# Optimization experiments

Hardware: AMD Instinct MI355X
Metric: run time of the kernel (lower is better)

## Reference

```python
import jax, jax.numpy as jnp
import numpy as np

NEG = -1e9  # effectively -inf for masked logits, grad-safe

def apply_rope(t, cos, sin):
    # t: [b, H, S, D]; cos/sin: [S, D] -> rotate-half RoPE
    d = t.shape[-1]
    t1, t2 = t[..., : d // 2], t[..., d // 2 :]
    rot = jnp.concatenate([-t2, t1], axis=-1)
    return t * cos[None, None] + rot * sin[None, None]


def setup_inputs() -> dict:
    key = jax.random.key(0)
    ks = jax.random.split(key, 8)
    b, S, d_in = 1, 4096, 2048
    H, G, D = 16, 4, 128
    d_out = H * D
    sc = 1.0 / np.sqrt(d_in)
    x = jax.random.normal(ks[0], (b, S, d_in), dtype=jnp.float32)
    # causal mask: True = masked (future positions)
    mask = jnp.triu(jnp.ones((S, S), dtype=bool), k=1)
    inv = 1.0 / (10000.0 ** (jnp.arange(0, D, 2, dtype=jnp.float32) / D))
    ang = jnp.arange(S, dtype=jnp.float32)[:, None] * inv[None, :]  # [S, D/2]
    ang = jnp.concatenate([ang, ang], axis=-1)                      # [S, D]
    cos, sin = jnp.cos(ang), jnp.sin(ang)
    Wq = jax.random.normal(ks[1], (d_out, d_in), dtype=jnp.float32) * sc
    Wk = jax.random.normal(ks[2], (G * D, d_in), dtype=jnp.float32) * sc
    Wv = jax.random.normal(ks[3], (G * D, d_in), dtype=jnp.float32) * sc
    Wo = jax.random.normal(ks[4], (d_in, d_out), dtype=jnp.float32) * sc
    return {"x": x, "mask": mask, "cos": cos, "sin": sin,
            "Wq": Wq, "Wk": Wk, "Wv": Wv, "Wo": Wo}


def reference(x, mask, cos, sin, Wq, Wk, Wv, Wo):
    b, S, d_in = x.shape
    G = Wk.shape[0] // cos.shape[-1]          # num_kv_groups
    D = cos.shape[-1]                          # head_dim
    H = Wq.shape[0] // D                       # num_heads
    n = H // G                                 # group_size
    q = (x @ Wq.T).reshape(b, S, H, D).transpose(0, 2, 1, 3)   # [b,H,S,D]
    k = (x @ Wk.T).reshape(b, S, G, D).transpose(0, 2, 1, 3)   # [b,G,S,D]
    v = (x @ Wv.T).reshape(b, S, G, D).transpose(0, 2, 1, 3)
    q = apply_rope(q, cos, sin)
    k = apply_rope(k, cos, sin)
    # GQA: group heads instead of repeat_interleave (head h -> group h // n)
    qg = q.reshape(b, G, n, S, D)
    scores = jnp.einsum('bgnqd,bgkd->bgnqk', qg, k)            # [b,G,n,S,S]
    scores = jnp.where(mask[None, None, None], NEG, scores)
    w = jax.nn.softmax(scores / np.sqrt(D), axis=-1)
    ctx = jnp.einsum('bgnqk,bgkd->bgnqd', w, v)                # [b,G,n,S,D]
    ctx = ctx.reshape(b, H, S, D).transpose(0, 2, 1, 3).reshape(b, S, H * D)
    return ctx @ Wo.T
```

## Files before the change

### kernel.cpp

```cpp
#include <hip/hip_runtime.h>

typedef __attribute__((ext_vector_type(8))) short bf16x8;
typedef __attribute__((ext_vector_type(4))) short bf16x4;
typedef __attribute__((ext_vector_type(8))) unsigned short u16x8;
typedef __attribute__((ext_vector_type(4))) float f32x4;

__device__ __forceinline__ unsigned short f2b(float f) {
  unsigned int u = __builtin_bit_cast(unsigned int, f);
  u += 0x7FFFu + ((u >> 16) & 1u);
  return (unsigned short)(u >> 16);
}
__device__ __forceinline__ float b2f(unsigned short h) {
  return __builtin_bit_cast(float, ((unsigned int)h) << 16);
}

__device__ __forceinline__ f32x4 mfma16x16x16(bf16x4 a, bf16x4 b, f32x4 c) {
#if __has_builtin(__builtin_amdgcn_mfma_f32_16x16x16bf16_1k)
  return __builtin_amdgcn_mfma_f32_16x16x16bf16_1k(a, b, c, 0, 0, 0);
#else
  asm volatile("v_mfma_f32_16x16x16_bf16 %0, %1, %2, %0" : "+v"(c) : "v"(a), "v"(b));
  return c;
#endif
}

#define AS1(p) (const __attribute__((address_space(1))) void*)(p)
#define AS3(p) (__attribute__((address_space(3))) void*)(p)

__global__ __launch_bounds__(256) void k_cvt(const float* __restrict__ in,
                                             unsigned short* __restrict__ out,
                                             float scale) {
  int i = blockIdx.x * 256 + threadIdx.x;
  const float4* p = (const float4*)in + (size_t)i * 2;
  float4 a = p[0], b = p[1];
  u16x8 r;
  r[0] = f2b(a.x * scale); r[1] = f2b(a.y * scale);
  r[2] = f2b(a.z * scale); r[3] = f2b(a.w * scale);
  r[4] = f2b(b.x * scale); r[5] = f2b(b.y * scale);
  r[6] = f2b(b.z * scale); r[7] = f2b(b.w * scale);
  *((u16x8*)out + i) = r;
}

__global__ __launch_bounds__(256) void k_rope(unsigned short* __restrict__ qk,
                                              const float* __restrict__ cosb,
                                              const float* __restrict__ sinb) {
  int tid = blockIdx.x * 256 + threadIdx.x;
  int oct = tid & 7;
  int hd  = (tid >> 3) % 20;
  int s   = (tid >> 3) / 20;
  unsigned short* p1 = qk + (size_t)s * 3072 + hd * 128 + oct * 8;
  unsigned short* p2 = p1 + 64;
  u16x8 a = *(const u16x8*)p1;
  u16x8 b = *(const u16x8*)p2;
  const float4* cp = (const float4*)(cosb + (size_t)s * 128 + oct * 8);
  const float4* sp = (const float4*)(sinb + (size_t)s * 128 + oct * 8);
  float4 c0 = cp[0], c1 = cp[1], s0 = sp[0], s1 = sp[1];
  float cs[8] = {c0.x,c0.y,c0.z,c0.w,c1.x,c1.y,c1.z,c1.w};
  float sn[8] = {s0.x,s0.y,s0.z,s0.w,s1.x,s1.y,s1.z,s1.w};
  u16x8 ra, rb;
#pragma unroll
  for (int j = 0; j < 8; ++j) {
    float av = b2f(a[j]), bv = b2f(b[j]);
    ra[j] = f2b(av * cs[j] - bv * sn[j]);
    rb[j] = f2b(bv * cs[j] + av * sn[j]);
  }
  *(u16x8*)p1 = ra;
  *(u16x8*)p2 = rb;
}

__global__ __launch_bounds__(256) void k_tr(const unsigned short* __restrict__ src,
                                            unsigned short* __restrict__ dst) {
  __shared__ unsigned short tile[64][72];
  const int bs = blockIdx.x, bc = blockIdx.y, t = threadIdx.x;
#pragma unroll
  for (int i = 0; i < 2; ++i) {
    int c8 = t + 256 * i;
    int row = c8 >> 3, cb = c8 & 7;
    u16x8 v = *(const u16x8*)(src + (size_t)(bs * 64 + row) * 3072 + 2560 + bc * 64 + cb * 8);
#pragma unroll
    for (int j = 0; j < 8; ++j) tile[row][cb * 8 + j] = v[j];
  }
  __syncthreads();
#pragma unroll
  for (int i = 0; i < 2; ++i) {
    int c8 = t + 256 * i;
    int crow = c8 >> 3, sb = c8 & 7;
    u16x8 v;
#pragma unroll
    for (int j = 0; j < 8; ++j) v[j] = tile[sb * 8 + j][crow];
    *(u16x8*)(dst + (size_t)(bc * 64 + crow) * 4096 + bs * 64 + sb * 8) = v;
  }
}

template <int OUTF32>
__global__ __launch_bounds__(256) void k_gemm_bt(
    const unsigned short* __restrict__ A, const unsigned short* __restrict__ B,
    void* __restrict__ C, int K, int lda, int ldb, int ldc) {
  __shared__ unsigned short As[128 * 64];
  __shared__ unsigned short Bs[128 * 64];
  const int t = threadIdx.x;
  const int lane = t & 63, w = t >> 6;
  const int wm = w >> 1, wn = w & 1;
  const int bn = blockIdx.x, bm = blockIdx.y;
  const unsigned short* Arow = A + (size_t)(bm * 128) * lda;
  const unsigned short* Brow = B + (size_t)(bn * 128) * ldb;

  f32x4 acc[4][4] = {};
  for (int kt = 0; kt < K; kt += 64) {
#pragma unroll
    for (int i = 0; i < 4; ++i) {
      int idx = i * 256 + t;
      int r = idx >> 3, blk = idx & 7;
      int sb = blk ^ (r & 7);
      __builtin_amdgcn_global_load_lds(AS1(Arow + (size_t)r * lda + kt + sb * 8),
                                       AS3(As + (i * 256 + w * 64) * 8), 16, 0, 0);
    }
#pragma unroll
    for (int i = 0; i < 4; ++i) {
      int idx = i * 256 + t;
      int r = idx >> 3, blk = idx & 7;
      int sb = blk ^ (r & 7);
      __builtin_amdgcn_global_load_lds(AS1(Brow + (size_t)r * ldb + kt + sb * 8),
                                       AS3(Bs + (i * 256 + w * 64) * 8), 16, 0, 0);
    }
    __syncthreads();
#pragma unroll
    for (int kk = 0; kk < 2; ++kk) {
      bf16x8 av[4], bv[4];
#pragma unroll
      for (int i = 0; i < 4; ++i) {
        int r = wm * 64 + i * 16 + (lane & 15);
        int off = (r * 128 + (kk * 32 + (lane >> 4) * 8) * 2) ^ ((r & 7) << 4);
        av[i] = *(const bf16x8*)((const char*)As + off);
      }
#pragma unroll
      for (int j = 0; j < 4; ++j) {
        int r = wn * 64 + j * 16 + (lane & 15);
        int off = (r * 128 + (kk * 32 + (lane >> 4) * 8) * 2) ^ ((r & 7) << 4);
        bv[j] = *(const bf16x8*)((const char*)Bs + off);
      }
#pragma unroll
      for (int i = 0; i < 4; ++i)
#pragma unroll
        for (int j = 0; j < 4; ++j)
          acc[i][j] = __builtin_amdgcn_mfma_f32_16x16x32_bf16(av[i], bv[j], acc[i][j], 0, 0, 0);
    }
    __syncthreads();
  }
#pragma unroll
  for (int i = 0; i < 4; ++i)
#pragma unroll
    for (int j = 0; j < 4; ++j)
#pragma unroll
      for (int r = 0; r < 4; ++r) {
        int m = bm * 128 + wm * 64 + i * 16 + (lane >> 4) * 4 + r;
        int n = bn * 128 + wn * 64 + j * 16 + (lane & 15);
        float v = acc[i][j][r];
        if (OUTF32) ((float*)C)[(size_t)m * ldc + n] = v;
        else        ((unsigned short*)C)[(size_t)m * ldc + n] = f2b(v);
      }
}

__device__ __forceinline__ void stage_k(const unsigned short* __restrict__ qk,
                                        unsigned short* __restrict__ dst,
                                        int kt, int g, int t, int w) {
#pragma unroll
  for (int i = 0; i < 4; ++i) {
    int idx = i * 256 + t;
    int r = idx >> 4, blk = idx & 15;
    int sb = (blk & 8) | ((blk ^ r) & 7);
    __builtin_amdgcn_global_load_lds(
        AS1(qk + (size_t)(kt * 64 + r) * 3072 + 2048 + g * 128 + sb * 8),
        AS3(dst + (i * 256 + w * 64) * 8), 16, 0, 0);
  }
}
__device__ __forceinline__ void stage_v(const unsigned short* __restrict__ vT,
                                        unsigned short* __restrict__ dst,
                                        int kt, int g, int t, int w) {
#pragma unroll
  for (int i = 0; i < 4; ++i) {
    int idx = i * 256 + t;
    int r = idx >> 3, blk = idx & 7;
    int sb = blk ^ (r & 7);
    __builtin_amdgcn_global_load_lds(
        AS1(vT + (size_t)(g * 128 + r) * 4096 + kt * 64 + sb * 8),
        AS3(dst + (i * 256 + w * 64) * 8), 16, 0, 0);
  }
}

__global__ __launch_bounds__(256, 2) void k_attn(const unsigned short* __restrict__ qk,
                                                 const unsigned short* __restrict__ vT,
                                                 unsigned short* __restrict__ ctx) {
  __shared__ unsigned short Ks[2][64 * 128];
  __shared__ unsigned short Vs[2][64 * 128];
  const int b = blockIdx.x, h = blockIdx.y, g = h >> 2;
  const int t = threadIdx.x, lane = t & 63, w = t >> 6;
  const int l15 = lane & 15, lq = lane >> 4;

  for (int ph = 0; ph < 2; ++ph) {
    const int qt = ph ? 63 - b : b;
    const int qg = qt * 64 + w * 16 + l15;

    bf16x8 aq[4];
    {
      const unsigned short* qb =
          qk + (size_t)(qt * 64 + w * 16 + l15) * 3072 + h * 128 + lq * 8;
#pragma unroll
      for (int sl = 0; sl < 4; ++sl) aq[sl] = *(const bf16x8*)(qb + sl * 32);
    }
    f32x4 o[8] = {};
    float lsum = 0.f;

    stage_k(qk, Ks[0], 0, g, t, w);
    stage_v(vT, Vs[0], 0, g, t, w);
    asm volatile("s_waitcnt vmcnt(0)" ::: "memory");
    __builtin_amdgcn_s_barrier();

    auto tile = [&](const unsigned short* Kb, const unsigned short* Vb,
                    int kt, bool maskT) {
      f32x4 st[4] = {};
      __builtin_amdgcn_s_setprio(1);
#pragma unroll
      for (int sl = 0; sl < 4; ++sl)
#pragma unroll
        for (int nt = 0; nt < 4; ++nt) {
          int key = nt * 16 + l15;
          int off = (key * 256 + sl * 64 + lq * 16) ^ ((key & 7) << 4);
          bf16x8 bk = *(const bf16x8*)((const char*)Kb + off);
          st[nt] = __builtin_amdgcn_mfma_f32_16x16x32_bf16(bk, aq[sl], st[nt], 0, 0, 0);
        }
      __builtin_amdgcn_s_setprio(0);

      bf16x4 pa[4];
#pragma unroll
      for (int nt = 0; nt < 4; ++nt)
#pragma unroll
        for (int r = 0; r < 4; ++r) {
          float p = __builtin_amdgcn_exp2f(st[nt][r]);
          if (maskT) {
            int key = kt * 64 + nt * 16 + lq * 4 + r;
            if (key > qg) p = 0.f;
          }
          lsum += p;
          unsigned int u = __builtin_bit_cast(unsigned int, p) + 0x8000u;
          pa[nt][r] = (short)(u >> 16);
        }

      __builtin_amdgcn_s_setprio(1);
#pragma unroll
      for (int nt = 0; nt < 4; ++nt)
#pragma unroll
        for (int dt = 0; dt < 8; ++dt) {
          int d = dt * 16 + l15;
          int off = (d * 128 + nt * 32 + lq * 8) ^ ((d & 7) << 4);
          bf16x4 vv = *(const bf16x4*)((const char*)Vb + off);
          o[dt] = mfma16x16x16(pa[nt], vv, o[dt]);
        }
      __builtin_amdgcn_s_setprio(0);
    };

    for (int kt = 0; kt < qt; ++kt) {
      const int cur = kt & 1;
      stage_k(qk, Ks[cur ^ 1], kt + 1, g, t, w);
      stage_v(vT, Vs[cur ^ 1], kt + 1, g, t, w);
      tile(Ks[cur], Vs[cur], kt, false);
      asm volatile("s_waitcnt vmcnt(0)" ::: "memory");
      __builtin_amdgcn_s_barrier();
    }
    {
      const int cur = qt & 1;
      tile(Ks[cur], Vs[cur], qt, true);
      __builtin_amdgcn_s_barrier();
    }

    float fs = lsum;
    fs += __shfl_xor(fs, 16);
    fs += __shfl_xor(fs, 32);
    float invq[4];
#pragma unroll
    for (int r = 0; r < 4; ++r) invq[r] = 1.f / __shfl(fs, lq * 4 + r);
#pragma unroll
    for (int dt = 0; dt < 8; ++dt)
#pragma unroll
      for (int r = 0; r < 4; ++r) {
        int q = qt * 64 + w * 16 + lq * 4 + r;
        int c = h * 128 + dt * 16 + l15;
        ctx[(size_t)q * 2048 + c] = f2b(o[dt][r] * invq[r]);
      }
  }
}

extern "C" void kernel_launch(void* const* d_in, const int* in_sizes, int n_in,
                              void* d_out, int out_size, void* d_ws, size_t ws_size,
                              hipStream_t stream) {
  const float* x    = (const float*)d_in[0];
  const float* cosb = (const float*)d_in[2];
  const float* sinb = (const float*)d_in[3];
  const float* Wq   = (const float*)d_in[4];
  const float* Wk   = (const float*)d_in[5];
  const float* Wv   = (const float*)d_in[6];
  const float* Wo   = (const float*)d_in[7];

  char* p = (char*)d_ws;
  unsigned short* xb   = (unsigned short*)p; p += (size_t)8388608 * 2;
  unsigned short* wqkv = (unsigned short*)p; p += (size_t)6291456 * 2;
  unsigned short* Wob  = (unsigned short*)p; p += (size_t)4194304 * 2;
  unsigned short* qkvb = (unsigned short*)p; p += (size_t)4096 * 3072 * 2;
  unsigned short* vTb  = (unsigned short*)p; p += (size_t)512 * 4096 * 2;
  unsigned short* ctx  = (unsigned short*)p; p += (size_t)4096 * 2048 * 2;
  if (ws_size < (size_t)(p - (char*)d_ws)) return;

  const float SC = 0.12751741f;

  k_cvt<<<4096, 256, 0, stream>>>(x,  xb, 1.f);
  k_cvt<<<2048, 256, 0, stream>>>(Wq, wqkv,           SC);
  k_cvt<<< 512, 256, 0, stream>>>(Wk, wqkv + 4194304, 1.f);
  k_cvt<<< 512, 256, 0, stream>>>(Wv, wqkv + 5242880, 1.f);
  k_cvt<<<2048, 256, 0, stream>>>(Wo, Wob, 1.f);

  k_gemm_bt<0><<<dim3(24, 32), 256, 0, stream>>>(xb, wqkv, qkvb, 2048, 2048, 2048, 3072);

  k_rope<<<2560, 256, 0, stream>>>(qkvb, cosb, sinb);
  k_tr<<<dim3(64, 8), 256, 0, stream>>>(qkvb, vTb);

  k_attn<<<dim3(32, 16), 256, 0, stream>>>(qkvb, vTb, ctx);

  k_gemm_bt<1><<<dim3(16, 32), 256, 0, stream>>>(ctx, Wob, d_out, 2048, 2048, 2048, 2048);
}
```

Before: 255.1 us.

## Single-buffer V in attention, raise occupancy, and merge small prep kernels

The attention kernel drops the double-buffered V tile. Each V tile is now loaded after the P·V step and overlapped only with the next tile's QK and softmax, with split waitcnt and barrier points. This frees LDS so launch bounds can be raised to three blocks per CU. Separately, the five fp32→bf16 conversion launches become one kernel, and RoPE plus the V transpose become one launch, cutting launch overhead. The trade-off is less latency hiding for V loads, while a 512-block grid may not fill the extra occupancy.

Measured after the change: 276.1 us. 8.2% more time.

```diff
diff --git a/kernel.cpp b/kernel.cpp
--- a/kernel.cpp
+++ b/kernel.cpp
@@ -26,10 +26,9 @@
 #define AS1(p) (const __attribute__((address_space(1))) void*)(p)
 #define AS3(p) (__attribute__((address_space(3))) void*)(p)
 
-__global__ __launch_bounds__(256) void k_cvt(const float* __restrict__ in,
-                                             unsigned short* __restrict__ out,
-                                             float scale) {
-  int i = blockIdx.x * 256 + threadIdx.x;
+__device__ __forceinline__ void cvt8(const float* __restrict__ in,
+                                     unsigned short* __restrict__ out,
+                                     int i, float scale) {
   const float4* p = (const float4*)in + (size_t)i * 2;
   float4 a = p[0], b = p[1];
   u16x8 r;
@@ -40,54 +39,71 @@
   *((u16x8*)out + i) = r;
 }
 
-__global__ __launch_bounds__(256) void k_rope(unsigned short* __restrict__ qk,
+__global__ __launch_bounds__(256) void k_cvt_all(
+    const float* __restrict__ x,  const float* __restrict__ Wq,
+    const float* __restrict__ Wk, const float* __restrict__ Wv,
+    const float* __restrict__ Wo, unsigned short* __restrict__ xb,
+    unsigned short* __restrict__ wqkv, unsigned short* __restrict__ Wob,
+    float sc) {
+  int bid = blockIdx.x;
+  int tid = threadIdx.x;
+  if (bid < 4096)      cvt8(x,  xb,             (bid        ) * 256 + tid, 1.f);
+  else if (bid < 6144) cvt8(Wq, wqkv,           (bid - 4096) * 256 + tid, sc);
+  else if (bid < 6656) cvt8(Wk, wqkv + 4194304, (bid - 6144) * 256 + tid, 1.f);
+  else if (bid < 7168) cvt8(Wv, wqkv + 5242880, (bid - 6656) * 256 + tid, 1.f);
+  else                 cvt8(Wo, Wob,            (bid - 7168) * 256 + tid, 1.f);
+}
+
+__global__ __launch_bounds__(256) void k_post(unsigned short* __restrict__ qkv,
                                               const float* __restrict__ cosb,
-                                              const float* __restrict__ sinb) {
-  int tid = blockIdx.x * 256 + threadIdx.x;
-  int oct = tid & 7;
-  int hd  = (tid >> 3) % 20;
-  int s   = (tid >> 3) / 20;
-  unsigned short* p1 = qk + (size_t)s * 3072 + hd * 128 + oct * 8;
-  unsigned short* p2 = p1 + 64;
-  u16x8 a = *(const u16x8*)p1;
-  u16x8 b = *(const u16x8*)p2;
-  const float4* cp = (const float4*)(cosb + (size_t)s * 128 + oct * 8);
-  const float4* sp = (const float4*)(sinb + (size_t)s * 128 + oct * 8);
-  float4 c0 = cp[0], c1 = cp[1], s0 = sp[0], s1 = sp[1];
-  float cs[8] = {c0.x,c0.y,c0.z,c0.w,c1.x,c1.y,c1.z,c1.w};
-  float sn[8] = {s0.x,s0.y,s0.z,s0.w,s1.x,s1.y,s1.z,s1.w};
-  u16x8 ra, rb;
-#pragma unroll
-  for (int j = 0; j < 8; ++j) {
-    float av = b2f(a[j]), bv = b2f(b[j]);
-    ra[j] = f2b(av * cs[j] - bv * sn[j]);
-    rb[j] = f2b(bv * cs[j] + av * sn[j]);
-  }
-  *(u16x8*)p1 = ra;
-  *(u16x8*)p2 = rb;
-}
-
-__global__ __launch_bounds__(256) void k_tr(const unsigned short* __restrict__ src,
-                                            unsigned short* __restrict__ dst) {
+                                              const float* __restrict__ sinb,
+                                              unsigned short* __restrict__ vT) {
   __shared__ unsigned short tile[64][72];
-  const int bs = blockIdx.x, bc = blockIdx.y, t = threadIdx.x;
-#pragma unroll
-  for (int i = 0; i < 2; ++i) {
-    int c8 = t + 256 * i;
-    int row = c8 >> 3, cb = c8 & 7;
-    u16x8 v = *(const u16x8*)(src + (size_t)(bs * 64 + row) * 3072 + 2560 + bc * 64 + cb * 8);
-#pragma unroll
-    for (int j = 0; j < 8; ++j) tile[row][cb * 8 + j] = v[j];
-  }
-  __syncthreads();
-#pragma unroll
-  for (int i = 0; i < 2; ++i) {
-    int c8 = t + 256 * i;
-    int crow = c8 >> 3, sb = c8 & 7;
-    u16x8 v;
-#pragma unroll
-    for (int j = 0; j < 8; ++j) v[j] = tile[sb * 8 + j][crow];
-    *(u16x8*)(dst + (size_t)(bc * 64 + crow) * 4096 + bs * 64 + sb * 8) = v;
+  const int bid = blockIdx.x, t = threadIdx.x;
+  if (bid < 2560) {
+    int tid = bid * 256 + t;
+    int oct = tid & 7;
+    int hd  = (tid >> 3) % 20;
+    int s   = (tid >> 3) / 20;
+    unsigned short* p1 = qkv + (size_t)s * 3072 + hd * 128 + oct * 8;
+    unsigned short* p2 = p1 + 64;
+    u16x8 a = *(const u16x8*)p1;
+    u16x8 b = *(const u16x8*)p2;
+    const float4* cp = (const float4*)(cosb + (size_t)s * 128 + oct * 8);
+    const float4* sp = (const float4*)(sinb + (size_t)s * 128 + oct * 8);
+    float4 c0 = cp[0], c1 = cp[1], s0 = sp[0], s1 = sp[1];
+    float cs[8] = {c0.x,c0.y,c0.z,c0.w,c1.x,c1.y,c1.z,c1.w};
+    float sn[8] = {s0.x,s0.y,s0.z,s0.w,s1.x,s1.y,s1.z,s1.w};
+    u16x8 ra, rb;
+#pragma unroll
+    for (int j = 0; j < 8; ++j) {
+      float av = b2f(a[j]), bv = b2f(b[j]);
+      ra[j] = f2b(av * cs[j] - bv * sn[j]);
+      rb[j] = f2b(bv * cs[j] + av * sn[j]);
+    }
+    *(u16x8*)p1 = ra;
+    *(u16x8*)p2 = rb;
+  } else {
+    int idx = bid - 2560;
+    int bs = idx >> 3, bc = idx & 7;
+#pragma unroll
+    for (int i = 0; i < 2; ++i) {
+      int c8 = t + 256 * i;
+      int row = c8 >> 3, cb = c8 & 7;
+      u16x8 v = *(const u16x8*)(qkv + (size_t)(bs * 64 + row) * 3072 + 2560 + bc * 64 + cb * 8);
+#pragma unroll
+      for (int j = 0; j < 8; ++j) tile[row][cb * 8 + j] = v[j];
+    }
+    __syncthreads();
+#pragma unroll
+    for (int i = 0; i < 2; ++i) {
+      int c8 = t + 256 * i;
+      int crow = c8 >> 3, sb = c8 & 7;
+      u16x8 v;
+#pragma unroll
+      for (int j = 0; j < 8; ++j) v[j] = tile[sb * 8 + j][crow];
+      *(u16x8*)(vT + (size_t)(bc * 64 + crow) * 4096 + bs * 64 + sb * 8) = v;
+    }
   }
 }
 
@@ -187,11 +203,11 @@
   }
 }
 
-__global__ __launch_bounds__(256, 2) void k_attn(const unsigned short* __restrict__ qk,
+__global__ __launch_bounds__(256, 3) void k_attn(const unsigned short* __restrict__ qk,
                                                  const unsigned short* __restrict__ vT,
                                                  unsigned short* __restrict__ ctx) {
   __shared__ unsigned short Ks[2][64 * 128];
-  __shared__ unsigned short Vs[2][64 * 128];
+  __shared__ unsigned short Vs[64 * 128];
   const int b = blockIdx.x, h = blockIdx.y, g = h >> 2;
   const int t = threadIdx.x, lane = t & 63, w = t >> 6;
   const int l15 = lane & 15, lq = lane >> 4;
@@ -209,68 +225,77 @@
     }
     f32x4 o[8] = {};
     float lsum = 0.f;
+    bf16x4 pa[4];
 
     stage_k(qk, Ks[0], 0, g, t, w);
-    stage_v(vT, Vs[0], 0, g, t, w);
+    stage_v(vT, Vs, 0, g, t, w);
     asm volatile("s_waitcnt vmcnt(0)" ::: "memory");
     __builtin_amdgcn_s_barrier();
 
-    auto tile = [&](const unsigned short* Kb, const unsigned short* Vb,
-                    int kt, bool maskT) {
-      f32x4 st[4] = {};
-      __builtin_amdgcn_s_setprio(1);
-#pragma unroll
-      for (int sl = 0; sl < 4; ++sl)
-#pragma unroll
-        for (int nt = 0; nt < 4; ++nt) {
-          int key = nt * 16 + l15;
-          int off = (key * 256 + sl * 64 + lq * 16) ^ ((key & 7) << 4);
-          bf16x8 bk = *(const bf16x8*)((const char*)Kb + off);
-          st[nt] = __builtin_amdgcn_mfma_f32_16x16x32_bf16(bk, aq[sl], st[nt], 0, 0, 0);
-        }
-      __builtin_amdgcn_s_setprio(0);
-
-      bf16x4 pa[4];
-#pragma unroll
-      for (int nt = 0; nt < 4; ++nt)
-#pragma unroll
-        for (int r = 0; r < 4; ++r) {
-          float p = __builtin_amdgcn_exp2f(st[nt][r]);
-          if (maskT) {
-            int key = kt * 64 + nt * 16 + lq * 4 + r;
-            if (key > qg) p = 0.f;
-          }
-          lsum += p;
-          unsigned int u = __builtin_bit_cast(unsigned int, p) + 0x8000u;
-          pa[nt][r] = (short)(u >> 16);
-        }
-
-      __builtin_amdgcn_s_setprio(1);
-#pragma unroll
-      for (int nt = 0; nt < 4; ++nt)
-#pragma unroll
-        for (int dt = 0; dt < 8; ++dt) {
-          int d = dt * 16 + l15;
-          int off = (d * 128 + nt * 32 + lq * 8) ^ ((d & 7) << 4);
-          bf16x4 vv = *(const bf16x4*)((const char*)Vb + off);
-          o[dt] = mfma16x16x16(pa[nt], vv, o[dt]);
-        }
-      __builtin_amdgcn_s_setprio(0);
-    };
+#define QK_SM(KB, KT, MASKT)                                                   \
+    {                                                                          \
+      f32x4 st[4] = {};                                                        \
+      __builtin_amdgcn_s_setprio(1);                                           \
+      _Pragma("unroll")                                                        \
+      for (int sl = 0; sl < 4; ++sl)                                           \
+        _Pragma("unroll")                                                      \
+        for (int nt = 0; nt < 4; ++nt) {                                       \
+          int key = nt * 16 + l15;                                             \
+          int off = (key * 256 + sl * 64 + lq * 16) ^ ((key & 7) << 4);        \
+          bf16x8 bk = *(const bf16x8*)((const char*)(KB) + off);               \
+          st[nt] = __builtin_amdgcn_mfma_f32_16x16x32_bf16(bk, aq[sl], st[nt], 0, 0, 0); \
+        }                                                                      \
+      __builtin_amdgcn_s_setprio(0);                                           \
+      _Pragma("unroll")                                                        \
+      for (int nt = 0; nt < 4; ++nt)                                           \
+        _Pragma("unroll")                                                      \
+        for (int r = 0; r < 4; ++r) {                                          \
+          float pp = __builtin_amdgcn_exp2f(st[nt][r]);                        \
+          if (MASKT) {                                                         \
+            int key = (KT) * 64 + nt * 16 + lq * 4 + r;                        \
+            if (key > qg) pp = 0.f;                                            \
+          }                                                                    \
+          lsum += pp;                                                          \
+          unsigned int uu = __builtin_bit_cast(unsigned int, pp) + 0x8000u;    \
+          pa[nt][r] = (short)(uu >> 16);                                       \
+        }                                                                      \
+    }
+
+#define PV()                                                                   \
+    {                                                                          \
+      __builtin_amdgcn_s_setprio(1);                                           \
+      _Pragma("unroll")                                                        \
+      for (int nt = 0; nt < 4; ++nt)                                           \
+        _Pragma("unroll")                                                      \
+        for (int dt = 0; dt < 8; ++dt) {                                       \
+          int d = dt * 16 + l15;                                               \
+          int off = (d * 128 + nt * 32 + lq * 8) ^ ((d & 7) << 4);             \
+          bf16x4 vv = *(const bf16x4*)((const char*)Vs + off);                 \
+          o[dt] = mfma16x16x16(pa[nt], vv, o[dt]);                             \
+        }                                                                      \
+      __builtin_amdgcn_s_setprio(0);                                           \
+    }
 
     for (int kt = 0; kt < qt; ++kt) {
       const int cur = kt & 1;
       stage_k(qk, Ks[cur ^ 1], kt + 1, g, t, w);
-      stage_v(vT, Vs[cur ^ 1], kt + 1, g, t, w);
-      tile(Ks[cur], Vs[cur], kt, false);
+      QK_SM(Ks[cur], kt, false)
+      asm volatile("s_waitcnt vmcnt(4)" ::: "memory");
+      __builtin_amdgcn_s_barrier();
+      PV()
       asm volatile("s_waitcnt vmcnt(0)" ::: "memory");
       __builtin_amdgcn_s_barrier();
+      stage_v(vT, Vs, kt + 1, g, t, w);
     }
     {
-      const int cur = qt & 1;
-      tile(Ks[cur], Vs[cur], qt, true);
+      QK_SM(Ks[qt & 1], qt, true)
+      asm volatile("s_waitcnt vmcnt(0)" ::: "memory");
       __builtin_amdgcn_s_barrier();
-    }
+      PV()
+      __builtin_amdgcn_s_barrier();
+    }
+#undef QK_SM
+#undef PV
 
     float fs = lsum;
     fs += __shfl_xor(fs, 16);
@@ -311,16 +336,11 @@
 
   const float SC = 0.12751741f;
 
-  k_cvt<<<4096, 256, 0, stream>>>(x,  xb, 1.f);
-  k_cvt<<<2048, 256, 0, stream>>>(Wq, wqkv,           SC);
-  k_cvt<<< 512, 256, 0, stream>>>(Wk, wqkv + 4194304, 1.f);
-  k_cvt<<< 512, 256, 0, stream>>>(Wv, wqkv + 5242880, 1.f);
-  k_cvt<<<2048, 256, 0, stream>>>(Wo, Wob, 1.f);
+  k_cvt_all<<<9216, 256, 0, stream>>>(x, Wq, Wk, Wv, Wo, xb, wqkv, Wob, SC);
 
   k_gemm_bt<0><<<dim3(24, 32), 256, 0, stream>>>(xb, wqkv, qkvb, 2048, 2048, 2048, 3072);
 
-  k_rope<<<2560, 256, 0, stream>>>(qkvb, cosb, sinb);
-  k_tr<<<dim3(64, 8), 256, 0, stream>>>(qkvb, vTb);
+  k_post<<<3072, 256, 0, stream>>>(qkvb, cosb, sinb, vTb);
 
   k_attn<<<dim3(32, 16), 256, 0, stream>>>(qkvb, vTb, ctx);
 
```

## Process two heads per attention block and merge small prep kernels

Applied to the files above, without the earlier changes.

The attention kernel now gives each workgroup two query heads from the same KV group. Each staged K/V tile feeds twice the MFMA work, which halves the grid and the global/LDS traffic for K and V. Launch bounds drop to one block per SM and register use per thread roughly doubles, trading occupancy for reuse. Separately, the five conversion launches become one kernel, and RoPE plus the V transpose become one kernel, to cut launch overhead.

Result: slower. 263.6 us (+3.3%).

```diff
diff --git a/kernel.cpp b/kernel.cpp
--- a/kernel.cpp
+++ b/kernel.cpp
@@ -26,10 +26,9 @@
 #define AS1(p) (const __attribute__((address_space(1))) void*)(p)
 #define AS3(p) (__attribute__((address_space(3))) void*)(p)
 
-__global__ __launch_bounds__(256) void k_cvt(const float* __restrict__ in,
-                                             unsigned short* __restrict__ out,
-                                             float scale) {
-  int i = blockIdx.x * 256 + threadIdx.x;
+__device__ __forceinline__ void cvt8(const float* __restrict__ in,
+                                     unsigned short* __restrict__ out,
+                                     int i, float scale) {
   const float4* p = (const float4*)in + (size_t)i * 2;
   float4 a = p[0], b = p[1];
   u16x8 r;
@@ -40,54 +39,71 @@
   *((u16x8*)out + i) = r;
 }
 
-__global__ __launch_bounds__(256) void k_rope(unsigned short* __restrict__ qk,
+__global__ __launch_bounds__(256) void k_cvt_all(
+    const float* __restrict__ x,  const float* __restrict__ Wq,
+    const float* __restrict__ Wk, const float* __restrict__ Wv,
+    const float* __restrict__ Wo, unsigned short* __restrict__ xb,
+    unsigned short* __restrict__ wqkv, unsigned short* __restrict__ Wob,
+    float sc) {
+  int bid = blockIdx.x;
+  int tid = threadIdx.x;
+  if (bid < 4096)      cvt8(x,  xb,             (bid        ) * 256 + tid, 1.f);
+  else if (bid < 6144) cvt8(Wq, wqkv,           (bid - 4096) * 256 + tid, sc);
+  else if (bid < 6656) cvt8(Wk, wqkv + 4194304, (bid - 6144) * 256 + tid, 1.f);
+  else if (bid < 7168) cvt8(Wv, wqkv + 5242880, (bid - 6656) * 256 + tid, 1.f);
+  else                 cvt8(Wo, Wob,            (bid - 7168) * 256 + tid, 1.f);
+}
+
+__global__ __launch_bounds__(256) void k_post(unsigned short* __restrict__ qkv,
                                               const float* __restrict__ cosb,
-                                              const float* __restrict__ sinb) {
-  int tid = blockIdx.x * 256 + threadIdx.x;
-  int oct = tid & 7;
-  int hd  = (tid >> 3) % 20;
-  int s   = (tid >> 3) / 20;
-  unsigned short* p1 = qk + (size_t)s * 3072 + hd * 128 + oct * 8;
-  unsigned short* p2 = p1 + 64;
-  u16x8 a = *(const u16x8*)p1;
-  u16x8 b = *(const u16x8*)p2;
-  const float4* cp = (const float4*)(cosb + (size_t)s * 128 + oct * 8);
-  const float4* sp = (const float4*)(sinb + (size_t)s * 128 + oct * 8);
-  float4 c0 = cp[0], c1 = cp[1], s0 = sp[0], s1 = sp[1];
-  float cs[8] = {c0.x,c0.y,c0.z,c0.w,c1.x,c1.y,c1.z,c1.w};
-  float sn[8] = {s0.x,s0.y,s0.z,s0.w,s1.x,s1.y,s1.z,s1.w};
-  u16x8 ra, rb;
-#pragma unroll
-  for (int j = 0; j < 8; ++j) {
-    float av = b2f(a[j]), bv = b2f(b[j]);
-    ra[j] = f2b(av * cs[j] - bv * sn[j]);
-    rb[j] = f2b(bv * cs[j] + av * sn[j]);
-  }
-  *(u16x8*)p1 = ra;
-  *(u16x8*)p2 = rb;
-}
-
-__global__ __launch_bounds__(256) void k_tr(const unsigned short* __restrict__ src,
-                                            unsigned short* __restrict__ dst) {
+                                              const float* __restrict__ sinb,
+                                              unsigned short* __restrict__ vT) {
   __shared__ unsigned short tile[64][72];
-  const int bs = blockIdx.x, bc = blockIdx.y, t = threadIdx.x;
-#pragma unroll
-  for (int i = 0; i < 2; ++i) {
-    int c8 = t + 256 * i;
-    int row = c8 >> 3, cb = c8 & 7;
-    u16x8 v = *(const u16x8*)(src + (size_t)(bs * 64 + row) * 3072 + 2560 + bc * 64 + cb * 8);
-#pragma unroll
-    for (int j = 0; j < 8; ++j) tile[row][cb * 8 + j] = v[j];
-  }
-  __syncthreads();
-#pragma unroll
-  for (int i = 0; i < 2; ++i) {
-    int c8 = t + 256 * i;
-    int crow = c8 >> 3, sb = c8 & 7;
-    u16x8 v;
-#pragma unroll
-    for (int j = 0; j < 8; ++j) v[j] = tile[sb * 8 + j][crow];
-    *(u16x8*)(dst + (size_t)(bc * 64 + crow) * 4096 + bs * 64 + sb * 8) = v;
+  const int bid = blockIdx.x, t = threadIdx.x;
+  if (bid < 2560) {
+    int tid = bid * 256 + t;
+    int oct = tid & 7;
+    int hd  = (tid >> 3) % 20;
+    int s   = (tid >> 3) / 20;
+    unsigned short* p1 = qkv + (size_t)s * 3072 + hd * 128 + oct * 8;
+    unsigned short* p2 = p1 + 64;
+    u16x8 a = *(const u16x8*)p1;
+    u16x8 b = *(const u16x8*)p2;
+    const float4* cp = (const float4*)(cosb + (size_t)s * 128 + oct * 8);
+    const float4* sp = (const float4*)(sinb + (size_t)s * 128 + oct * 8);
+    float4 c0 = cp[0], c1 = cp[1], s0 = sp[0], s1 = sp[1];
+    float cs[8] = {c0.x,c0.y,c0.z,c0.w,c1.x,c1.y,c1.z,c1.w};
+    float sn[8] = {s0.x,s0.y,s0.z,s0.w,s1.x,s1.y,s1.z,s1.w};
+    u16x8 ra, rb;
+#pragma unroll
+    for (int j = 0; j < 8; ++j) {
+      float av = b2f(a[j]), bv = b2f(b[j]);
+      ra[j] = f2b(av * cs[j] - bv * sn[j]);
+      rb[j] = f2b(bv * cs[j] + av * sn[j]);
+    }
+    *(u16x8*)p1 = ra;
+    *(u16x8*)p2 = rb;
+  } else {
+    int idx = bid - 2560;
+    int bs = idx >> 3, bc = idx & 7;
+#pragma unroll
+    for (int i = 0; i < 2; ++i) {
+      int c8 = t + 256 * i;
+      int row = c8 >> 3, cb = c8 & 7;
+      u16x8 v = *(const u16x8*)(qkv + (size_t)(bs * 64 + row) * 3072 + 2560 + bc * 64 + cb * 8);
+#pragma unroll
+      for (int j = 0; j < 8; ++j) tile[row][cb * 8 + j] = v[j];
+    }
+    __syncthreads();
+#pragma unroll
+    for (int i = 0; i < 2; ++i) {
+      int c8 = t + 256 * i;
+      int crow = c8 >> 3, sb = c8 & 7;
+      u16x8 v;
+#pragma unroll
+      for (int j = 0; j < 8; ++j) v[j] = tile[sb * 8 + j][crow];
+      *(u16x8*)(vT + (size_t)(bc * 64 + crow) * 4096 + bs * 64 + sb * 8) = v;
+    }
   }
 }
 
@@ -187,12 +203,14 @@
   }
 }
 
-__global__ __launch_bounds__(256, 2) void k_attn(const unsigned short* __restrict__ qk,
+__global__ __launch_bounds__(256, 1) void k_attn(const unsigned short* __restrict__ qk,
                                                  const unsigned short* __restrict__ vT,
                                                  unsigned short* __restrict__ ctx) {
   __shared__ unsigned short Ks[2][64 * 128];
   __shared__ unsigned short Vs[2][64 * 128];
-  const int b = blockIdx.x, h = blockIdx.y, g = h >> 2;
+  const int b = blockIdx.x;
+  const int hp = blockIdx.y;
+  const int h0 = hp * 2, g = hp >> 1;
   const int t = threadIdx.x, lane = t & 63, w = t >> 6;
   const int l15 = lane & 15, lq = lane >> 4;
 
@@ -200,15 +218,18 @@
     const int qt = ph ? 63 - b : b;
     const int qg = qt * 64 + w * 16 + l15;
 
-    bf16x8 aq[4];
+    bf16x8 aq0[4], aq1[4];
     {
       const unsigned short* qb =
-          qk + (size_t)(qt * 64 + w * 16 + l15) * 3072 + h * 128 + lq * 8;
-#pragma unroll
-      for (int sl = 0; sl < 4; ++sl) aq[sl] = *(const bf16x8*)(qb + sl * 32);
-    }
-    f32x4 o[8] = {};
-    float lsum = 0.f;
+          qk + (size_t)(qt * 64 + w * 16 + l15) * 3072 + h0 * 128 + lq * 8;
+#pragma unroll
+      for (int sl = 0; sl < 4; ++sl) {
+        aq0[sl] = *(const bf16x8*)(qb + sl * 32);
+        aq1[sl] = *(const bf16x8*)(qb + 128 + sl * 32);
+      }
+    }
+    f32x4 o0[8] = {}, o1[8] = {};
+    float lsum0 = 0.f, lsum1 = 0.f;
 
     stage_k(qk, Ks[0], 0, g, t, w);
     stage_v(vT, Vs[0], 0, g, t, w);
@@ -217,7 +238,7 @@
 
     auto tile = [&](const unsigned short* Kb, const unsigned short* Vb,
                     int kt, bool maskT) {
-      f32x4 st[4] = {};
+      f32x4 st0[4] = {}, st1[4] = {};
       __builtin_amdgcn_s_setprio(1);
 #pragma unroll
       for (int sl = 0; sl < 4; ++sl)
@@ -226,23 +247,27 @@
           int key = nt * 16 + l15;
           int off = (key * 256 + sl * 64 + lq * 16) ^ ((key & 7) << 4);
           bf16x8 bk = *(const bf16x8*)((const char*)Kb + off);
-          st[nt] = __builtin_amdgcn_mfma_f32_16x16x32_bf16(bk, aq[sl], st[nt], 0, 0, 0);
+          st0[nt] = __builtin_amdgcn_mfma_f32_16x16x32_bf16(bk, aq0[sl], st0[nt], 0, 0, 0);
+          st1[nt] = __builtin_amdgcn_mfma_f32_16x16x32_bf16(bk, aq1[sl], st1[nt], 0, 0, 0);
         }
       __builtin_amdgcn_s_setprio(0);
 
-      bf16x4 pa[4];
+      bf16x4 pa0[4], pa1[4];
 #pragma unroll
       for (int nt = 0; nt < 4; ++nt)
 #pragma unroll
         for (int r = 0; r < 4; ++r) {
-          float p = __builtin_amdgcn_exp2f(st[nt][r]);
+          float p0 = __builtin_amdgcn_exp2f(st0[nt][r]);
+          float p1 = __builtin_amdgcn_exp2f(st1[nt][r]);
           if (maskT) {
             int key = kt * 64 + nt * 16 + lq * 4 + r;
-            if (key > qg) p = 0.f;
+            if (key > qg) { p0 = 0.f; p1 = 0.f; }
           }
-          lsum += p;
-          unsigned int u = __builtin_bit_cast(unsigned int, p) + 0x8000u;
-          pa[nt][r] = (short)(u >> 16);
+          lsum0 += p0; lsum1 += p1;
+          unsigned int u0 = __builtin_bit_cast(unsigned int, p0) + 0x8000u;
+          unsigned int u1 = __builtin_bit_cast(unsigned int, p1) + 0x8000u;
+          pa0[nt][r] = (short)(u0 >> 16);
+          pa1[nt][r] = (short)(u1 >> 16);
         }
 
       __builtin_amdgcn_s_setprio(1);
@@ -253,7 +278,8 @@
           int d = dt * 16 + l15;
           int off = (d * 128 + nt * 32 + lq * 8) ^ ((d & 7) << 4);
           bf16x4 vv = *(const bf16x4*)((const char*)Vb + off);
-          o[dt] = mfma16x16x16(pa[nt], vv, o[dt]);
+          o0[dt] = mfma16x16x16(pa0[nt], vv, o0[dt]);
+          o1[dt] = mfma16x16x16(pa1[nt], vv, o1[dt]);
         }
       __builtin_amdgcn_s_setprio(0);
     };
@@ -267,24 +293,27 @@
       __builtin_amdgcn_s_barrier();
     }
     {
-      const int cur = qt & 1;
-      tile(Ks[cur], Vs[cur], qt, true);
+      tile(Ks[qt & 1], Vs[qt & 1], qt, true);
       __builtin_amdgcn_s_barrier();
     }
 
-    float fs = lsum;
-    fs += __shfl_xor(fs, 16);
-    fs += __shfl_xor(fs, 32);
-    float invq[4];
-#pragma unroll
-    for (int r = 0; r < 4; ++r) invq[r] = 1.f / __shfl(fs, lq * 4 + r);
+    float f0 = lsum0, f1 = lsum1;
+    f0 += __shfl_xor(f0, 16); f0 += __shfl_xor(f0, 32);
+    f1 += __shfl_xor(f1, 16); f1 += __shfl_xor(f1, 32);
+    float iq0[4], iq1[4];
+#pragma unroll
+    for (int r = 0; r < 4; ++r) {
+      iq0[r] = 1.f / __shfl(f0, lq * 4 + r);
+      iq1[r] = 1.f / __shfl(f1, lq * 4 + r);
+    }
 #pragma unroll
     for (int dt = 0; dt < 8; ++dt)
 #pragma unroll
       for (int r = 0; r < 4; ++r) {
         int q = qt * 64 + w * 16 + lq * 4 + r;
-        int c = h * 128 + dt * 16 + l15;
-        ctx[(size_t)q * 2048 + c] = f2b(o[dt][r] * invq[r]);
+        int c = h0 * 128 + dt * 16 + l15;
+        ctx[(size_t)q * 2048 + c]       = f2b(o0[dt][r] * iq0[r]);
+        ctx[(size_t)q * 2048 + c + 128] = f2b(o1[dt][r] * iq1[r]);
       }
   }
 }
@@ -311,18 +340,13 @@
 
   const float SC = 0.12751741f;
 
-  k_cvt<<<4096, 256, 0, stream>>>(x,  xb, 1.f);
-  k_cvt<<<2048, 256, 0, stream>>>(Wq, wqkv,           SC);
-  k_cvt<<< 512, 256, 0, stream>>>(Wk, wqkv + 4194304, 1.f);
-  k_cvt<<< 512, 256, 0, stream>>>(Wv, wqkv + 5242880, 1.f);
-  k_cvt<<<2048, 256, 0, stream>>>(Wo, Wob, 1.f);
+  k_cvt_all<<<9216, 256, 0, stream>>>(x, Wq, Wk, Wv, Wo, xb, wqkv, Wob, SC);
 
   k_gemm_bt<0><<<dim3(24, 32), 256, 0, stream>>>(xb, wqkv, qkvb, 2048, 2048, 2048, 3072);
 
-  k_rope<<<2560, 256, 0, stream>>>(qkvb, cosb, sinb);
-  k_tr<<<dim3(64, 8), 256, 0, stream>>>(qkvb, vTb);
-
-  k_attn<<<dim3(32, 16), 256, 0, stream>>>(qkvb, vTb, ctx);
+  k_post<<<3072, 256, 0, stream>>>(qkvb, cosb, sinb, vTb);
+
+  k_attn<<<dim3(32, 8), 256, 0, stream>>>(qkvb, vTb, ctx);
 
   k_gemm_bt<1><<<dim3(16, 32), 256, 0, stream>>>(ctx, Wob, d_out, 2048, 2048, 2048, 2048);
 }
```
